# Kernel optimization log

Hardware: AMD Instinct MI355X
Metric: run time of the kernel (lower is better)

The kernel has to match this reference:

```python
import jax, jax.numpy as jnp
import numpy as np

B, K, D, C = 8192, 16, 1024, 512


def setup_inputs() -> dict:
    key = jax.random.key(0)
    k1, k2, k3, k4, k5 = jax.random.split(key, 5)
    concepts = jax.random.normal(k1, (B, K, D), dtype=jnp.float32)
    slot_ids = jax.random.randint(k2, (B,), 0, K)
    labels = jax.random.randint(k3, (B,), 0, C)
    # per-slot Linear(concept_dim -> num_classes): weight (K, C, D), bias (K, C)
    W = jax.random.normal(k4, (K, C, D), dtype=jnp.float32) / np.sqrt(D).astype(np.float32)
    bias = jax.random.normal(k5, (K, C), dtype=jnp.float32) * 0.01
    return {"concepts": concepts, "slot_ids": slot_ids, "labels": labels, "W": W, "bias": bias}


def reference(concepts, slot_ids, labels, W, bias):
    # Each example b uses slot s=slot_ids[b]: logits = concepts[b, s, :] @ W[s].T + bias[s].
    # Vectorized as K batched GEMMs over the slot axis, then gather the relevant row.
    logits = jnp.einsum('bkd,kcd->bkc', concepts, W) + bias  # (B, K, C)
    logp = jax.nn.log_softmax(logits, axis=-1)
    bidx = jnp.arange(concepts.shape[0])
    ce = -logp[bidx, slot_ids, labels]  # per-example cross entropy (B,)
    nK = W.shape[0]
    counts = jax.ops.segment_sum(jnp.ones_like(ce), slot_ids, num_segments=nK)
    sums = jax.ops.segment_sum(ce, slot_ids, num_segments=nK)
    means = sums / jnp.maximum(counts, 1.0)          # per-slot mean CE (= F.cross_entropy per group)
    present = counts > 0
    n_present = jnp.maximum(jnp.sum(present), 1)     # torch: count of unique slots, max(count,1)
    return jnp.sum(jnp.where(present, means, 0.0)) / n_present
```

## Files before the change

kernel.cpp:

```cpp
#include <hip/hip_runtime.h>
#include <hip/hip_bf16.h>

#define B_N 8192
#define K_N 16
#define D_N 1024
#define C_N 512
#define BM  32

typedef __bf16 bf16x8 __attribute__((ext_vector_type(8)));
typedef float  f32x4  __attribute__((ext_vector_type(4)));
typedef float  f32x4v __attribute__((ext_vector_type(4)));
typedef unsigned int u32x4 __attribute__((ext_vector_type(4)));
typedef unsigned int u32x2 __attribute__((ext_vector_type(2)));

static __device__ __forceinline__ unsigned short f2bf(float f) {
    union { float f; unsigned int u; } x; x.f = f;
    unsigned int r = x.u + 0x7FFFu + ((x.u >> 16) & 1u);
    return (unsigned short)(r >> 16);
}

static __device__ __forceinline__ bf16x8 load_bf8(const unsigned short* p) {
    union { u32x4 u; bf16x8 v; } t;
    t.u = *(const u32x4*)p;
    return t.v;
}

static __device__ __forceinline__ bf16x8 zero_bf8() {
    union { u32x4 u; bf16x8 v; } t;
    u32x4 z = {0u, 0u, 0u, 0u};
    t.u = z;
    return t.v;
}


__global__ void initk(int* counts, int* cursors, float* ce_sums) {
    int t = threadIdx.x;
    if (t < K_N) { counts[t] = 0; cursors[t] = 0; ce_sums[t] = 0.f; }
}

__global__ void countk(const int* __restrict__ slot_ids, int* __restrict__ counts) {
    __shared__ int h[K_N];
    if (threadIdx.x < K_N) h[threadIdx.x] = 0;
    __syncthreads();
    for (int b = blockIdx.x * blockDim.x + threadIdx.x; b < B_N; b += gridDim.x * blockDim.x)
        atomicAdd(&h[slot_ids[b]], 1);
    __syncthreads();
    if (threadIdx.x < K_N) atomicAdd(&counts[threadIdx.x], h[threadIdx.x]);
}

__global__ void scank(const int* __restrict__ counts, int* __restrict__ offsets) {
    if (threadIdx.x == 0 && blockIdx.x == 0) {
        int a = 0;
        for (int s = 0; s < K_N; ++s) { offsets[s] = a; a += counts[s]; }
    }
}

__global__ void scatterk(const int* __restrict__ slot_ids, const int* __restrict__ labels,
                         const int* __restrict__ offsets, int* __restrict__ cursors,
                         int* __restrict__ order_rows, int* __restrict__ lab_g) {
    for (int b = blockIdx.x * blockDim.x + threadIdx.x; b < B_N; b += gridDim.x * blockDim.x) {
        int s = slot_ids[b];
        int p = atomicAdd(&cursors[s], 1);
        int idx = offsets[s] + p;
        order_rows[idx] = b * K_N + s;
        lab_g[idx] = labels[b];
    }
}

__global__ void convw(const float* __restrict__ W, unsigned short* __restrict__ Wb) {
    int i = (blockIdx.x * 256 + threadIdx.x) * 8;
    f32x4v a = *(const f32x4v*)(W + i);
    f32x4v b = *(const f32x4v*)(W + i + 4);
    u32x4 o;
    o[0] = (unsigned)f2bf(a[0]) | ((unsigned)f2bf(a[1]) << 16);
    o[1] = (unsigned)f2bf(a[2]) | ((unsigned)f2bf(a[3]) << 16);
    o[2] = (unsigned)f2bf(b[0]) | ((unsigned)f2bf(b[1]) << 16);
    o[3] = (unsigned)f2bf(b[2]) | ((unsigned)f2bf(b[3]) << 16);
    *(u32x4*)(Wb + i) = o;
}

__global__ void gatherx(const float* __restrict__ concepts, const int* __restrict__ order_rows,
                        unsigned short* __restrict__ Xg) {
    int idx = blockIdx.x;
    int row = order_rows[idx];
    const float* in = concepts + (size_t)row * D_N;
    unsigned short* out = Xg + (size_t)idx * D_N;
    int t = threadIdx.x * 4;
    f32x4v a = *(const f32x4v*)(in + t);
    u32x2 o;
    o[0] = (unsigned)f2bf(a[0]) | ((unsigned)f2bf(a[1]) << 16);
    o[1] = (unsigned)f2bf(a[2]) | ((unsigned)f2bf(a[3]) << 16);
    *(u32x2*)(out + t) = o;
}

__global__ __launch_bounds__(256) void gemm_ce(
        const unsigned short* __restrict__ Xg, const unsigned short* __restrict__ Wb,
        const float* __restrict__ bias, const int* __restrict__ counts,
        const int* __restrict__ offsets, const int* __restrict__ lab_g,
        float* __restrict__ ce_sums) {
    int s = blockIdx.y;
    int cnt = counts[s];
    int row0 = blockIdx.x * BM;
    if (row0 >= cnt) return;
    int nrows = min(BM, cnt - row0);
    int base = offsets[s];

    int tid = threadIdx.x;
    int wave = tid >> 6, lane = tid & 63;
    int col = lane & 15, quad = lane >> 4;
    int c0 = wave * 128;

    f32x4 acc[2][8];
    f32x4 zf = {0.f, 0.f, 0.f, 0.f};
#pragma unroll
    for (int m = 0; m < 2; ++m)
#pragma unroll
        for (int t = 0; t < 8; ++t) acc[m][t] = zf;

    const unsigned short* aptr[2];
    bool avalid[2];
#pragma unroll
    for (int m = 0; m < 2; ++m) {
        int lr = m * 16 + col;
        avalid[m] = lr < nrows;
        int gr = base + row0 + (avalid[m] ? lr : 0);
        aptr[m] = Xg + (size_t)gr * D_N + quad * 8;
    }
    const unsigned short* bptr = Wb + ((size_t)s * C_N + c0 + col) * D_N + quad * 8;

    for (int k = 0; k < D_N; k += 32) {
        bf16x8 af[2];
#pragma unroll
        for (int m = 0; m < 2; ++m)
            af[m] = avalid[m] ? load_bf8(aptr[m] + k) : zero_bf8();
        bf16x8 bfr[8];
#pragma unroll
        for (int t = 0; t < 8; ++t)
            bfr[t] = load_bf8(bptr + (size_t)t * 16 * D_N + k);
#pragma unroll
        for (int m = 0; m < 2; ++m)
#pragma unroll
            for (int t = 0; t < 8; ++t)
                acc[m][t] = __builtin_amdgcn_mfma_f32_16x16x32_bf16(af[m], bfr[t], acc[m][t], 0, 0, 0);
    }

    __shared__ float smax[4][BM];
    __shared__ float ssum[4][BM];
    __shared__ float gmax[BM];
    __shared__ float slab[BM];

#pragma unroll
    for (int t = 0; t < 8; ++t) {
        float bv = bias[(size_t)s * C_N + c0 + t * 16 + col];
#pragma unroll
        for (int m = 0; m < 2; ++m)
#pragma unroll
            for (int r = 0; r < 4; ++r) acc[m][t][r] += bv;
    }

#pragma unroll
    for (int m = 0; m < 2; ++m)
#pragma unroll
        for (int r = 0; r < 4; ++r) {
            float v = acc[m][0][r];
#pragma unroll
            for (int t = 1; t < 8; ++t) v = fmaxf(v, acc[m][t][r]);
            v = fmaxf(v, __shfl_xor(v, 1, 64));
            v = fmaxf(v, __shfl_xor(v, 2, 64));
            v = fmaxf(v, __shfl_xor(v, 4, 64));
            v = fmaxf(v, __shfl_xor(v, 8, 64));
            if (col == 0) smax[wave][m * 16 + quad * 4 + r] = v;
        }
    __syncthreads();
    if (tid < BM)
        gmax[tid] = fmaxf(fmaxf(smax[0][tid], smax[1][tid]),
                          fmaxf(smax[2][tid], smax[3][tid]));
    __syncthreads();

#pragma unroll
    for (int m = 0; m < 2; ++m)
#pragma unroll
        for (int r = 0; r < 4; ++r) {
            int row = m * 16 + quad * 4 + r;
            float gm = gmax[row];
            int lab = (row < nrows) ? lab_g[base + row0 + row] : -1;
            float sv = 0.f;
#pragma unroll
            for (int t = 0; t < 8; ++t) {
                float x = acc[m][t][r];
                sv += __expf(x - gm);
                if (c0 + t * 16 + col == lab) slab[row] = x;
            }
            sv += __shfl_xor(sv, 1, 64);
            sv += __shfl_xor(sv, 2, 64);
            sv += __shfl_xor(sv, 4, 64);
            sv += __shfl_xor(sv, 8, 64);
            if (col == 0) ssum[wave][row] = sv;
        }
    __syncthreads();

    if (wave == 0) {
        float ce = 0.f;
        if (lane < nrows) {
            float gs = ssum[0][lane] + ssum[1][lane] + ssum[2][lane] + ssum[3][lane];
            ce = gmax[lane] + __logf(gs) - slab[lane];
        }
        ce += __shfl_xor(ce, 1, 64);
        ce += __shfl_xor(ce, 2, 64);
        ce += __shfl_xor(ce, 4, 64);
        ce += __shfl_xor(ce, 8, 64);
        ce += __shfl_xor(ce, 16, 64);
        ce += __shfl_xor(ce, 32, 64);
        if (lane == 0) atomicAdd(&ce_sums[s], ce);
    }
}

__global__ void finalize(const int* __restrict__ counts, const float* __restrict__ ce_sums,
                         float* __restrict__ out) {
    if (threadIdx.x == 0 && blockIdx.x == 0) {
        float tot = 0.f; int np = 0;
        for (int s = 0; s < K_N; ++s) {
            int c = counts[s];
            if (c > 0) { tot += ce_sums[s] / (float)c; np++; }
        }
        out[0] = tot / (float)(np > 0 ? np : 1);
    }
}

extern "C" void kernel_launch(void* const* d_in, const int* in_sizes, int n_in,
                              void* d_out, int out_size, void* d_ws, size_t ws_size,
                              hipStream_t stream) {
    const float* concepts = (const float*)d_in[0];
    const int*   slot_ids = (const int*)d_in[1];
    const int*   labels   = (const int*)d_in[2];
    const float* W        = (const float*)d_in[3];
    const float* bias     = (const float*)d_in[4];
    float* out = (float*)d_out;

    char* ws = (char*)d_ws;
    int*   counts     = (int*)(ws + 0);
    int*   offsets    = (int*)(ws + 64);
    int*   cursors    = (int*)(ws + 128);
    float* ce_sums    = (float*)(ws + 192);
    int*   order_rows = (int*)(ws + 256);
    int*   lab_g      = (int*)(ws + 256 + 4 * B_N);
    unsigned short* Wb = (unsigned short*)(ws + 131072);
    unsigned short* Xg = (unsigned short*)(ws + 131072 + (size_t)2 * K_N * C_N * D_N);

    initk<<<1, 64, 0, stream>>>(counts, cursors, ce_sums);
    countk<<<32, 256, 0, stream>>>(slot_ids, counts);
    scank<<<1, 1, 0, stream>>>(counts, offsets);
    scatterk<<<32, 256, 0, stream>>>(slot_ids, labels, offsets, cursors, order_rows, lab_g);
    convw<<<(K_N * C_N * D_N) / (256 * 8), 256, 0, stream>>>(W, Wb);
    gatherx<<<B_N, 256, 0, stream>>>(concepts, order_rows, Xg);
    gemm_ce<<<dim3(B_N / BM, K_N), 256, 0, stream>>>(Xg, Wb, bias, counts, offsets, lab_g, ce_sums);
    finalize<<<1, 1, 0, stream>>>(counts, ce_sums, out);
}
```

Baseline: 745.3 us.

## Fuse gather/convert into GEMM and merge setup kernels into fewer launches

Removes the separate gatherx pass that wrote a bf16 copy of the selected concept rows. The GEMM now indexes through order_rows, reads the fp32 concept rows directly and packs them to bf16 in registers. The four small setup kernels become a single-block histogram/scan kernel, and the weight conversion and scatter run in one combined launch. This cuts kernel launches and an intermediate round trip through memory, but the GEMM now loads fp32 A data, twice the bytes, does conversion work inside the inner loop, and pads partial tiles with clamped duplicate rows.

```diff
diff --git a/kernel.cpp b/kernel.cpp
--- a/kernel.cpp
+++ b/kernel.cpp
@@ -6,12 +6,14 @@
 #define D_N 1024
 #define C_N 512
 #define BM  32
+#define CONVW_BLOCKS 4096
+#define SCATTER_BLOCKS 32
 
 typedef __bf16 bf16x8 __attribute__((ext_vector_type(8)));
+typedef __bf16 bf16x2 __attribute__((ext_vector_type(2)));
 typedef float  f32x4  __attribute__((ext_vector_type(4)));
 typedef float  f32x4v __attribute__((ext_vector_type(4)));
 typedef unsigned int u32x4 __attribute__((ext_vector_type(4)));
-typedef unsigned int u32x2 __attribute__((ext_vector_type(2)));
 
 static __device__ __forceinline__ unsigned short f2bf(float f) {
     union { float f; unsigned int u; } x; x.f = f;
@@ -19,85 +21,81 @@
     return (unsigned short)(r >> 16);
 }
 
+static __device__ __forceinline__ bf16x2 pk2(float x, float y) {
+#if __has_builtin(__builtin_amdgcn_cvt_pk_bf16_f32)
+    return __builtin_amdgcn_cvt_pk_bf16_f32(x, y);
+#else
+    union { unsigned int u; bf16x2 v; } t;
+    t.u = (unsigned)f2bf(x) | ((unsigned)f2bf(y) << 16);
+    return t.v;
+#endif
+}
+
+static __device__ __forceinline__ bf16x8 cvt8(f32x4v a, f32x4v b) {
+    bf16x2 p0 = pk2(a[0], a[1]), p1 = pk2(a[2], a[3]);
+    bf16x2 p2 = pk2(b[0], b[1]), p3 = pk2(b[2], b[3]);
+    bf16x8 r;
+    r[0] = p0[0]; r[1] = p0[1]; r[2] = p1[0]; r[3] = p1[1];
+    r[4] = p2[0]; r[5] = p2[1]; r[6] = p3[0]; r[7] = p3[1];
+    return r;
+}
+
 static __device__ __forceinline__ bf16x8 load_bf8(const unsigned short* p) {
     union { u32x4 u; bf16x8 v; } t;
     t.u = *(const u32x4*)p;
     return t.v;
 }
 
-static __device__ __forceinline__ bf16x8 zero_bf8() {
-    union { u32x4 u; bf16x8 v; } t;
-    u32x4 z = {0u, 0u, 0u, 0u};
-    t.u = z;
-    return t.v;
-}
-
-
-__global__ void initk(int* counts, int* cursors, float* ce_sums) {
+__global__ void histk(const int* __restrict__ slot_ids, int* __restrict__ counts,
+                      int* __restrict__ offsets, int* __restrict__ cursors,
+                      float* __restrict__ ce_sums) {
+    __shared__ int h[K_N];
     int t = threadIdx.x;
-    if (t < K_N) { counts[t] = 0; cursors[t] = 0; ce_sums[t] = 0.f; }
-}
-
-__global__ void countk(const int* __restrict__ slot_ids, int* __restrict__ counts) {
-    __shared__ int h[K_N];
-    if (threadIdx.x < K_N) h[threadIdx.x] = 0;
-    __syncthreads();
-    for (int b = blockIdx.x * blockDim.x + threadIdx.x; b < B_N; b += gridDim.x * blockDim.x)
-        atomicAdd(&h[slot_ids[b]], 1);
-    __syncthreads();
-    if (threadIdx.x < K_N) atomicAdd(&counts[threadIdx.x], h[threadIdx.x]);
-}
-
-__global__ void scank(const int* __restrict__ counts, int* __restrict__ offsets) {
-    if (threadIdx.x == 0 && blockIdx.x == 0) {
+    if (t < K_N) h[t] = 0;
+    __syncthreads();
+    for (int b = t; b < B_N; b += 1024) atomicAdd(&h[slot_ids[b]], 1);
+    __syncthreads();
+    if (t == 0) {
         int a = 0;
-        for (int s = 0; s < K_N; ++s) { offsets[s] = a; a += counts[s]; }
-    }
-}
-
-__global__ void scatterk(const int* __restrict__ slot_ids, const int* __restrict__ labels,
-                         const int* __restrict__ offsets, int* __restrict__ cursors,
-                         int* __restrict__ order_rows, int* __restrict__ lab_g) {
-    for (int b = blockIdx.x * blockDim.x + threadIdx.x; b < B_N; b += gridDim.x * blockDim.x) {
-        int s = slot_ids[b];
-        int p = atomicAdd(&cursors[s], 1);
-        int idx = offsets[s] + p;
-        order_rows[idx] = b * K_N + s;
-        lab_g[idx] = labels[b];
-    }
-}
-
-__global__ void convw(const float* __restrict__ W, unsigned short* __restrict__ Wb) {
-    int i = (blockIdx.x * 256 + threadIdx.x) * 8;
-    f32x4v a = *(const f32x4v*)(W + i);
-    f32x4v b = *(const f32x4v*)(W + i + 4);
-    u32x4 o;
-    o[0] = (unsigned)f2bf(a[0]) | ((unsigned)f2bf(a[1]) << 16);
-    o[1] = (unsigned)f2bf(a[2]) | ((unsigned)f2bf(a[3]) << 16);
-    o[2] = (unsigned)f2bf(b[0]) | ((unsigned)f2bf(b[1]) << 16);
-    o[3] = (unsigned)f2bf(b[2]) | ((unsigned)f2bf(b[3]) << 16);
-    *(u32x4*)(Wb + i) = o;
-}
-
-__global__ void gatherx(const float* __restrict__ concepts, const int* __restrict__ order_rows,
-                        unsigned short* __restrict__ Xg) {
-    int idx = blockIdx.x;
-    int row = order_rows[idx];
-    const float* in = concepts + (size_t)row * D_N;
-    unsigned short* out = Xg + (size_t)idx * D_N;
-    int t = threadIdx.x * 4;
-    f32x4v a = *(const f32x4v*)(in + t);
-    u32x2 o;
-    o[0] = (unsigned)f2bf(a[0]) | ((unsigned)f2bf(a[1]) << 16);
-    o[1] = (unsigned)f2bf(a[2]) | ((unsigned)f2bf(a[3]) << 16);
-    *(u32x2*)(out + t) = o;
+        for (int s = 0; s < K_N; ++s) {
+            int c = h[s];
+            counts[s] = c; offsets[s] = a; cursors[s] = a; ce_sums[s] = 0.f;
+            a += c;
+        }
+    }
+}
+
+__global__ void prep(const float* __restrict__ W, unsigned short* __restrict__ Wb,
+                     const int* __restrict__ slot_ids, const int* __restrict__ labels,
+                     int* __restrict__ cursors, int* __restrict__ order_rows,
+                     int* __restrict__ lab_g) {
+    int bid = blockIdx.x;
+    if (bid < CONVW_BLOCKS) {
+        size_t i = ((size_t)bid * 256 + threadIdx.x) * 8;
+        f32x4v a = *(const f32x4v*)(W + i);
+        f32x4v b = *(const f32x4v*)(W + i + 4);
+        u32x4 o;
+        o[0] = (unsigned)f2bf(a[0]) | ((unsigned)f2bf(a[1]) << 16);
+        o[1] = (unsigned)f2bf(a[2]) | ((unsigned)f2bf(a[3]) << 16);
+        o[2] = (unsigned)f2bf(b[0]) | ((unsigned)f2bf(b[1]) << 16);
+        o[3] = (unsigned)f2bf(b[2]) | ((unsigned)f2bf(b[3]) << 16);
+        *(u32x4*)(Wb + i) = o;
+    } else {
+        int b0 = bid - CONVW_BLOCKS;
+        for (int b = b0 * 256 + threadIdx.x; b < B_N; b += SCATTER_BLOCKS * 256) {
+            int s = slot_ids[b];
+            int idx = atomicAdd(&cursors[s], 1);
+            order_rows[idx] = b * K_N + s;
+            lab_g[idx] = labels[b];
+        }
+    }
 }
 
 __global__ __launch_bounds__(256) void gemm_ce(
-        const unsigned short* __restrict__ Xg, const unsigned short* __restrict__ Wb,
+        const float* __restrict__ concepts, const unsigned short* __restrict__ Wb,
         const float* __restrict__ bias, const int* __restrict__ counts,
-        const int* __restrict__ offsets, const int* __restrict__ lab_g,
-        float* __restrict__ ce_sums) {
+        const int* __restrict__ offsets, const int* __restrict__ order_rows,
+        const int* __restrict__ lab_g, float* __restrict__ ce_sums) {
     int s = blockIdx.y;
     int cnt = counts[s];
     int row0 = blockIdx.x * BM;
@@ -117,22 +115,23 @@
 #pragma unroll
         for (int t = 0; t < 8; ++t) acc[m][t] = zf;
 
-    const unsigned short* aptr[2];
-    bool avalid[2];
+    const float* aptr[2];
 #pragma unroll
     for (int m = 0; m < 2; ++m) {
-        int lr = m * 16 + col;
-        avalid[m] = lr < nrows;
-        int gr = base + row0 + (avalid[m] ? lr : 0);
-        aptr[m] = Xg + (size_t)gr * D_N + quad * 8;
+        int lr = min(m * 16 + col, nrows - 1);
+        int orow = order_rows[base + row0 + lr];
+        aptr[m] = concepts + (size_t)orow * D_N + quad * 8;
     }
     const unsigned short* bptr = Wb + ((size_t)s * C_N + c0 + col) * D_N + quad * 8;
 
     for (int k = 0; k < D_N; k += 32) {
         bf16x8 af[2];
 #pragma unroll
-        for (int m = 0; m < 2; ++m)
-            af[m] = avalid[m] ? load_bf8(aptr[m] + k) : zero_bf8();
+        for (int m = 0; m < 2; ++m) {
+            f32x4v x0 = *(const f32x4v*)(aptr[m] + k);
+            f32x4v x1 = *(const f32x4v*)(aptr[m] + k + 4);
+            af[m] = cvt8(x0, x1);
+        }
         bf16x8 bfr[8];
 #pragma unroll
         for (int t = 0; t < 8; ++t)
@@ -245,14 +244,11 @@
     int*   order_rows = (int*)(ws + 256);
     int*   lab_g      = (int*)(ws + 256 + 4 * B_N);
     unsigned short* Wb = (unsigned short*)(ws + 131072);
-    unsigned short* Xg = (unsigned short*)(ws + 131072 + (size_t)2 * K_N * C_N * D_N);
-
-    initk<<<1, 64, 0, stream>>>(counts, cursors, ce_sums);
-    countk<<<32, 256, 0, stream>>>(slot_ids, counts);
-    scank<<<1, 1, 0, stream>>>(counts, offsets);
-    scatterk<<<32, 256, 0, stream>>>(slot_ids, labels, offsets, cursors, order_rows, lab_g);
-    convw<<<(K_N * C_N * D_N) / (256 * 8), 256, 0, stream>>>(W, Wb);
-    gatherx<<<B_N, 256, 0, stream>>>(concepts, order_rows, Xg);
-    gemm_ce<<<dim3(B_N / BM, K_N), 256, 0, stream>>>(Xg, Wb, bias, counts, offsets, lab_g, ce_sums);
+
+    histk<<<1, 1024, 0, stream>>>(slot_ids, counts, offsets, cursors, ce_sums);
+    prep<<<CONVW_BLOCKS + SCATTER_BLOCKS, 256, 0, stream>>>(W, Wb, slot_ids, labels,
+                                                            cursors, order_rows, lab_g);
+    gemm_ce<<<dim3(B_N / BM, K_N), 256, 0, stream>>>(concepts, Wb, bias, counts, offsets,
+                                                     order_rows, lab_g, ce_sums);
     finalize<<<1, 1, 0, stream>>>(counts, ce_sums, out);
 }
```

Result: no change. 752.8 us (+1.0%).
